# Performance work log

Measured on AMD Instinct MI355X. Metric: run time of the kernel, lower is better.

The kernel has to match this reference:

```python
import jax, jax.numpy as jnp
import numpy as np

D = 1024      # embedding_dimension
F = 4096      # intermediate_dimension
E = 8         # num_experts
K = 2         # top_k
B, S = 4, 2048


def setup_inputs() -> dict:
    key = jax.random.key(0)
    ks = jax.random.split(key, 6)
    scale_in = 1.0 / np.sqrt(D)
    scale_mid = 1.0 / np.sqrt(F)
    return {
        "x": jax.random.normal(ks[0], (B, S, D), dtype=jnp.float32),
        "router_w": jax.random.normal(ks[1], (E, D), dtype=jnp.float32) * scale_in,   # nn.Linear weight [out,in]
        "w1": jax.random.normal(ks[2], (E, F, D), dtype=jnp.float32) * scale_in,
        "b1": jax.random.normal(ks[3], (E, F), dtype=jnp.float32) * 0.01,
        "w2": jax.random.normal(ks[4], (E, D, F), dtype=jnp.float32) * scale_mid,
        "b2": jax.random.normal(ks[5], (E, D), dtype=jnp.float32) * 0.01,
    }


def reference(x, router_w, w1, b1, w2, b2):
    orig_shape = x.shape
    xf = x.reshape(-1, D)                                  # [T, D]
    logits = jnp.einsum("td,ed->te", xf, router_w)        # [T, E]
    top_vals, top_idx = jax.lax.top_k(logits, K)           # [T, K]
    probs = jax.nn.softmax(top_vals, axis=-1)              # [T, K]

    out = jnp.zeros_like(xf)
    for e in range(E):  # small fixed expert loop; masked dense combine
        # combine weight per token for expert e (0 if not routed)
        w = jnp.sum(jnp.where(top_idx == e, probs, 0.0), axis=-1)   # [T]
        h = jax.nn.gelu(jnp.einsum("td,fd->tf", xf, w1[e]) + b1[e], approximate=False)
        y = jnp.einsum("tf,df->td", h, w2[e]) + b2[e]
        out = out + w[:, None] * y
    return out.reshape(orig_shape)
```

## Files before the change

kernel.cpp:

```cpp
#include <hip/hip_runtime.h>
#include <hip/hip_bf16.h>
#include <stdint.h>

#define D 1024
#define F 4096
#define E 8
#define T 8192
#define SLOT_CAP 18432
#define BM 128
#define BK 32
#define EP_STRIDE 136

#define BM2 256
#define BN2 256
#define BK2 32
#define EP2 268

typedef __attribute__((ext_vector_type(8))) short bf16x8;
typedef __attribute__((ext_vector_type(4))) float f32x4;
typedef __attribute__((ext_vector_type(8))) unsigned short u16x8;

__device__ __forceinline__ unsigned short f2bf(float f) {
  unsigned u = __float_as_uint(f);
  u += 0x7fffu + ((u >> 16) & 1u);
  return (unsigned short)(u >> 16);
}
__device__ __forceinline__ float bf2f(unsigned short u) {
  return __uint_as_float(((unsigned)u) << 16);
}

__device__ __forceinline__ float gelu_f(float v) {
  float s = fabsf(v) * 0.70710678118654752f;
  float t = __builtin_amdgcn_rcpf(fmaf(0.3275911f, s, 1.0f));
  float p = fmaf(t, 1.061405429f, -1.453152027f);
  p = fmaf(t, p, 1.421413741f);
  p = fmaf(t, p, -0.284496736f);
  p = fmaf(t, p, 0.254829592f);
  p = p * t;
  float e = 1.0f - p * __expf(-s * s);
  e = copysignf(e, v);
  return 0.5f * v * (1.0f + e);
}

__device__ __forceinline__ void gload16(const void* g, void* l) {
  auto gp = (const __attribute__((address_space(1))) unsigned int*)(uintptr_t)g;
  auto lp = (__attribute__((address_space(3))) unsigned int*)(unsigned)(uintptr_t)l;
  __builtin_amdgcn_global_load_lds(gp, lp, 16, 0, 0);
}

__global__ __launch_bounds__(256) void prep_kernel(const float* __restrict__ x,
                                                   const float* __restrict__ rw,
                                                   const float* __restrict__ w1,
                                                   const float* __restrict__ w2,
                                                   int* __restrict__ tok_e,
                                                   float* __restrict__ tok_p,
                                                   unsigned short* __restrict__ xg,
                                                   unsigned short* __restrict__ w1g,
                                                   unsigned short* __restrict__ w2g) {
  if (blockIdx.x >= 2048) {
    const int n8 = E * F * D / 8;
    int i = (blockIdx.x - 2048) * 256 + threadIdx.x;
    const float* in = w1;
    unsigned short* out = w1g;
    if (i >= n8) { i -= n8; in = w2; out = w2g; }
    const float4* p = (const float4*)in + (size_t)i * 2;
    float4 a = p[0], b = p[1];
    u16x8 o;
    o[0] = f2bf(a.x); o[1] = f2bf(a.y); o[2] = f2bf(a.z); o[3] = f2bf(a.w);
    o[4] = f2bf(b.x); o[5] = f2bf(b.y); o[6] = f2bf(b.z); o[7] = f2bf(b.w);
    *(u16x8*)(out + (size_t)i * 8) = o;
    return;
  }
  int t = blockIdx.x * 4 + (threadIdx.x >> 6);
  int lane = threadIdx.x & 63;
  const float* xp = x + (size_t)t * D;
  unsigned short* xgp = xg + (size_t)t * D;
  double acc[E];
#pragma unroll
  for (int e = 0; e < E; e++) acc[e] = 0.0;
  for (int j = 0; j < D / 64; j++) {
    float xv = xp[j * 64 + lane];
    xgp[j * 64 + lane] = f2bf(xv);
#pragma unroll
    for (int e = 0; e < E; e++) acc[e] += (double)xv * (double)rw[e * D + j * 64 + lane];
  }
#pragma unroll
  for (int e = 0; e < E; e++) {
#pragma unroll
    for (int off = 32; off >= 1; off >>= 1) acc[e] += __shfl_xor(acc[e], off, 64);
  }
  if (lane == 0) {
    double v0 = -1e300, v1 = -1e300;
    int i0 = 0, i1 = 0;
#pragma unroll
    for (int e = 0; e < E; e++) {
      double v = acc[e];
      if (v > v0) { v1 = v0; i1 = i0; v0 = v; i0 = e; }
      else if (v > v1) { v1 = v; i1 = e; }
    }
    double e1 = exp(v1 - v0);
    double s = 1.0 + e1;
    tok_e[2 * t] = i0; tok_e[2 * t + 1] = i1;
    tok_p[2 * t] = (float)(1.0 / s);
    tok_p[2 * t + 1] = (float)(e1 / s);
  }
}

__global__ __launch_bounds__(64) void bucket_kernel(const int* __restrict__ tok_e,
                                                    int* __restrict__ perm,
                                                    int* __restrict__ slot_of,
                                                    int* __restrict__ counts,
                                                    int* __restrict__ offp) {
  const int e = blockIdx.x;
  const int lane = threadIdx.x;
  int cnt[E];
#pragma unroll
  for (int ee = 0; ee < E; ee++) cnt[ee] = 0;
  for (int idx = lane; idx < 2 * T; idx += 64) {
    int v = tok_e[idx];
#pragma unroll
    for (int ee = 0; ee < E; ee++) cnt[ee] += (v == ee) ? 1 : 0;
  }
#pragma unroll
  for (int ee = 0; ee < E; ee++) {
#pragma unroll
    for (int off = 32; off >= 1; off >>= 1) cnt[ee] += __shfl_xor(cnt[ee], off, 64);
  }
  int off_e[E + 1];
  int o = 0;
#pragma unroll
  for (int ee = 0; ee < E; ee++) { off_e[ee] = o; o += (cnt[ee] + 255) & ~255; }
  off_e[E] = o;
  if (e == 0 && lane == 0) {
#pragma unroll
    for (int ee = 0; ee < E; ee++) { counts[ee] = cnt[ee]; offp[ee] = off_e[ee]; }
    offp[E] = o;
  }
  int base = 0, mycnt = 0, myend = 0;
#pragma unroll
  for (int ee = 0; ee < E; ee++) {
    if (ee == e) { base = off_e[ee]; mycnt = cnt[ee]; myend = off_e[ee + 1]; }
  }
  const int pad0 = base + mycnt;
  for (int r = 0; r < 2 * T / 64; r++) {
    int idx = r * 64 + lane;
    int v = tok_e[idx];
    bool m = (v == e);
    unsigned long long mask = __ballot(m);
    int pre = __popcll(mask & ((1ull << lane) - 1ull));
    if (m) {
      int slot = base + pre;
      perm[slot] = idx >> 1;
      slot_of[idx] = slot;
    }
    base += __popcll(mask);
  }
  for (int i = pad0 + lane; i < myend; i += 64) perm[i] = 0;
}

__global__ __launch_bounds__(512, 2) void gemm1_kernel(const unsigned short* __restrict__ xg,
                                                       const unsigned short* __restrict__ w1g,
                                                       const float* __restrict__ b1,
                                                       const int* __restrict__ perm,
                                                       const int* __restrict__ offp,
                                                       const int* __restrict__ counts,
                                                       unsigned short* __restrict__ hbuf) {
  const int id = blockIdx.x;
  const int swz = (id & 7) * 144 + (id >> 3);
  const int bm = swz >> 4, bn = swz & 15;
  const int row0 = bm * BM2;
  if (row0 >= offp[E]) return;
  int e = 0;
#pragma unroll
  for (int i = 0; i < E; i++) if (row0 >= offp[i + 1]) e = i + 1;
  if (row0 >= offp[e] + counts[e]) return;

  const int t = threadIdx.x, lane = t & 63, w = t >> 6;
  const int wm = w >> 2, wn = w & 3;
  const int fr = lane & 15, fq = lane >> 4;

  __shared__ __align__(16) unsigned short smem[65536];

  const int srow = t >> 2;
  const int c = (t & 3) ^ (srow & 3);
  const unsigned short* srcA[2];
  const unsigned short* srcB[2];
  {
    int p0 = perm[row0 + srow], p1 = perm[row0 + 128 + srow];
    srcA[0] = xg + (size_t)p0 * D + c * 8;
    srcA[1] = xg + (size_t)p1 * D + c * 8;
    srcB[0] = w1g + ((size_t)e * F + (size_t)bn * BN2 + srow) * D + c * 8;
    srcB[1] = w1g + ((size_t)e * F + (size_t)bn * BN2 + 128 + srow) * D + c * 8;
  }

  float biasv[4];
#pragma unroll
  for (int n = 0; n < 4; n++) {
    biasv[n] = b1[e * F + bn * BN2 + wn * 64 + n * 16 + fr];
    asm volatile("" :: "v"(biasv[n]));
  }

  auto stageA = [&](int tk) {
    unsigned short* base = smem + (tk & 3) * 16384 + t * 8;
    gload16(srcA[0] + tk * 32, base);
    gload16(srcA[1] + tk * 32, base + 4096);
  };
  auto stageB = [&](int tk) {
    unsigned short* base = smem + (tk & 3) * 16384 + 8192 + t * 8;
    gload16(srcB[0] + tk * 32, base);
    gload16(srcB[1] + tk * 32, base + 4096);
  };

  int aoff[8], boff[4];
#pragma unroll
  for (int m = 0; m < 8; m++) {
    int row = wm * 128 + m * 16 + fr;
    aoff[m] = row * 32 + ((fq ^ (row & 3)) * 8);
  }
#pragma unroll
  for (int n = 0; n < 4; n++) {
    int row = wn * 64 + n * 16 + fr;
    boff[n] = 8192 + row * 32 + ((fq ^ (row & 3)) * 8);
  }

  f32x4 acc[8][4] = {};

  stageA(0); stageB(0);
  stageA(1); stageB(1);
  stageA(2); stageB(2);
  asm volatile("s_waitcnt vmcnt(8)" ::: "memory");
  __builtin_amdgcn_s_barrier();
  __builtin_amdgcn_sched_barrier(0);

  const int NK = D / BK2;
#pragma unroll 4
  for (int kt = 0; kt < NK; ++kt) {
    const unsigned short* tb = smem + (kt & 3) * 16384;
    bf16x8 a0[4], b[4];
#pragma unroll
    for (int m = 0; m < 4; m++) a0[m] = *(const bf16x8*)(tb + aoff[m]);
#pragma unroll
    for (int n = 0; n < 4; n++) b[n] = *(const bf16x8*)(tb + boff[n]);
    if (kt + 3 < NK) stageA(kt + 3);
    __builtin_amdgcn_s_setprio(1);
#pragma unroll
    for (int m = 0; m < 4; m++)
#pragma unroll
      for (int n = 0; n < 4; n++)
        acc[m][n] = __builtin_amdgcn_mfma_f32_16x16x32_bf16(a0[m], b[n], acc[m][n], 0, 0, 0);
    __builtin_amdgcn_s_setprio(0);
    __builtin_amdgcn_s_barrier();
    __builtin_amdgcn_sched_barrier(0);
    bf16x8 a1[4];
#pragma unroll
    for (int m = 0; m < 4; m++) a1[m] = *(const bf16x8*)(tb + aoff[4 + m]);
    if (kt + 3 < NK) stageB(kt + 3);
    __builtin_amdgcn_s_setprio(1);
#pragma unroll
    for (int m = 0; m < 4; m++)
#pragma unroll
      for (int n = 0; n < 4; n++)
        acc[4 + m][n] = __builtin_amdgcn_mfma_f32_16x16x32_bf16(a1[m], b[n], acc[4 + m][n], 0, 0, 0);
    __builtin_amdgcn_s_setprio(0);
    if (kt < NK - 3)       { asm volatile("s_waitcnt vmcnt(8)" ::: "memory"); }
    else if (kt == NK - 3) { asm volatile("s_waitcnt vmcnt(4)" ::: "memory"); }
    else if (kt == NK - 2) { asm volatile("s_waitcnt vmcnt(0)" ::: "memory"); }
    __builtin_amdgcn_s_barrier();
    __builtin_amdgcn_sched_barrier(0);
  }

  __syncthreads();
  unsigned short* ep = smem;
#pragma unroll
  for (int p = 0; p < 2; p++) {
    if (wm == p) {
#pragma unroll
      for (int n = 0; n < 4; n++) {
        int col = wn * 64 + n * 16 + fr;
#pragma unroll
        for (int m = 0; m < 8; m++) {
#pragma unroll
          for (int j = 0; j < 4; j++) {
            int lr = m * 16 + fq * 4 + j;
            ep[lr * EP2 + col] = f2bf(gelu_f(acc[m][n][j] + biasv[n]));
          }
        }
      }
    }
    __syncthreads();
#pragma unroll
    for (int i = 0; i < 8; i++) {
      int idx = t + i * 512;
      int r2 = idx >> 5, c8 = (idx & 31) * 8;
      u16x8 v = *(const u16x8*)&ep[r2 * EP2 + c8];
      *(u16x8*)&hbuf[(size_t)(row0 + p * 128 + r2) * F + (size_t)bn * BN2 + c8] = v;
    }
    __syncthreads();
  }
}

__global__ __launch_bounds__(256, 3) void gemm2_kernel(const unsigned short* __restrict__ hbuf,
                                                       const unsigned short* __restrict__ w2g,
                                                       const float* __restrict__ b2,
                                                       const int* __restrict__ offp,
                                                       const int* __restrict__ counts,
                                                       unsigned short* __restrict__ ypart) {
  const int id = blockIdx.x;
  const int swz = (id & 7) * 288 + (id >> 3);
  const int bn = swz & 7;
  const int ks = (swz >> 3) & 1;
  const int bm = swz >> 4;
  const int row0 = bm * BM;
  if (row0 >= offp[E]) return;
  int e = 0;
#pragma unroll
  for (int i = 0; i < E; i++) if (row0 >= offp[i + 1]) e = i + 1;
  const int valid_end = offp[e] + counts[e];
  if (row0 >= valid_end) return;

  const int tid = threadIdx.x, lane = tid & 63, w = tid >> 6;
  __shared__ __align__(16) unsigned short smem[BM * EP_STRIDE];
  unsigned short* As0 = smem;
  unsigned short* Bs0 = smem + 8192;

  const int kbase = ks * (F / 2);
  const unsigned short* gsrc[4];
  unsigned short* ldst[4];
#pragma unroll
  for (int i = 0; i < 4; i++) {
    int ch = tid + 256 * i;
    if (ch < 512) {
      int ar = ch >> 2, ac = (ch & 3) * 8;
      gsrc[i] = hbuf + (size_t)(row0 + ar) * F + kbase + ac;
      ldst[i] = As0 + ch * 8;
    } else {
      int c = ch - 512;
      int br = c >> 2, bc = (c & 3) * 8;
      gsrc[i] = w2g + ((size_t)e * D + (size_t)bn * BM + br) * F + kbase + bc;
      ldst[i] = Bs0 + c * 8;
    }
  }
  auto stage = [&](int k0, int buf) {
#pragma unroll
    for (int i = 0; i < 4; i++) gload16(gsrc[i] + k0, ldst[i] + buf * (BM * BK));
  };

  f32x4 acc[4][4] = {};
  const int wr = (w >> 1) * 64, wc = (w & 1) * 64;
  const int fr = lane & 15, fq = lane >> 4;

  stage(0, 0);
  __syncthreads();
  int cur = 0;
  for (int k0 = 0; k0 < F / 2; k0 += BK) {
    if (k0 + BK < F / 2) stage(k0 + BK, cur ^ 1);
    bf16x8 a[4], b[4];
#pragma unroll
    for (int m = 0; m < 4; m++) a[m] = *(const bf16x8*)&As0[cur * 4096 + (wr + m * 16 + fr) * BK + fq * 8];
#pragma unroll
    for (int n = 0; n < 4; n++) b[n] = *(const bf16x8*)&Bs0[cur * 4096 + (wc + n * 16 + fr) * BK + fq * 8];
#pragma unroll
    for (int m = 0; m < 4; m++)
#pragma unroll
      for (int n = 0; n < 4; n++)
        acc[m][n] = __builtin_amdgcn_mfma_f32_16x16x32_bf16(a[m], b[n], acc[m][n], 0, 0, 0);
    __syncthreads();
    cur ^= 1;
  }

#pragma unroll
  for (int n = 0; n < 4; n++) {
    int cl = wc + n * 16 + fr;
    float bias = (ks == 0) ? b2[e * D + bn * BM + cl] : 0.0f;
#pragma unroll
    for (int m = 0; m < 4; m++) {
#pragma unroll
      for (int j = 0; j < 4; j++) {
        int rl = wr + m * 16 + fq * 4 + j;
        smem[rl * EP_STRIDE + cl] = f2bf(acc[m][n][j] + bias);
      }
    }
  }
  __syncthreads();
  unsigned short* ybase = ypart + (size_t)ks * SLOT_CAP * D;
#pragma unroll
  for (int i = 0; i < 8; i++) {
    int idx = tid + i * 256;
    int r2 = idx >> 4, c = (idx & 15) * 8;
    if (row0 + r2 < valid_end) {
      u16x8 v = *(const u16x8*)&smem[r2 * EP_STRIDE + c];
      *(u16x8*)&ybase[(size_t)(row0 + r2) * D + bn * BM + c] = v;
    }
  }
}

__global__ __launch_bounds__(256) void combine_kernel(const unsigned short* __restrict__ ypart,
                                                      const int* __restrict__ slot_of,
                                                      const float* __restrict__ tok_p,
                                                      float* __restrict__ out) {
  int i = blockIdx.x * 256 + threadIdx.x;
  int t = i >> 7;
  int g8 = i & 127;
  int s0 = slot_of[2 * t], s1 = slot_of[2 * t + 1];
  float g0 = tok_p[2 * t], g1 = tok_p[2 * t + 1];
  const unsigned short* p0 = ypart;
  const unsigned short* p1 = ypart + (size_t)SLOT_CAP * D;
  u16x8 a0 = *(const u16x8*)(p0 + (size_t)s0 * D + g8 * 8);
  u16x8 b0 = *(const u16x8*)(p1 + (size_t)s0 * D + g8 * 8);
  u16x8 a1 = *(const u16x8*)(p0 + (size_t)s1 * D + g8 * 8);
  u16x8 b1 = *(const u16x8*)(p1 + (size_t)s1 * D + g8 * 8);
  float o[8];
#pragma unroll
  for (int j = 0; j < 8; j++)
    o[j] = g0 * (bf2f(a0[j]) + bf2f(b0[j])) + g1 * (bf2f(a1[j]) + bf2f(b1[j]));
  float4* op = (float4*)(out + (size_t)t * D + g8 * 8);
  op[0] = make_float4(o[0], o[1], o[2], o[3]);
  op[1] = make_float4(o[4], o[5], o[6], o[7]);
}

extern "C" void kernel_launch(void* const* d_in, const int* in_sizes, int n_in,
                              void* d_out, int out_size, void* d_ws, size_t ws_size,
                              hipStream_t stream) {
  const float* x = (const float*)d_in[0];
  const float* rw = (const float*)d_in[1];
  const float* w1 = (const float*)d_in[2];
  const float* b1 = (const float*)d_in[3];
  const float* w2 = (const float*)d_in[4];
  const float* b2 = (const float*)d_in[5];
  float* out = (float*)d_out;

  char* ws = (char*)d_ws;
  size_t off = 0;
  auto alloc = [&](size_t bytes) {
    void* p = ws + off;
    off = (off + bytes + 255) & ~(size_t)255;
    return p;
  };
  int* counts = (int*)alloc(E * 4);
  int* offp = (int*)alloc((E + 1) * 4);
  int* tok_e = (int*)alloc((size_t)T * 2 * 4);
  float* tok_p = (float*)alloc((size_t)T * 2 * 4);
  int* perm = (int*)alloc((size_t)SLOT_CAP * 4);
  int* slot_of = (int*)alloc((size_t)T * 2 * 4);
  unsigned short* xg = (unsigned short*)alloc((size_t)T * D * 2);
  unsigned short* w1g = (unsigned short*)alloc((size_t)E * F * D * 2);
  unsigned short* w2g = (unsigned short*)alloc((size_t)E * D * F * 2);
  unsigned short* hbuf = (unsigned short*)alloc((size_t)SLOT_CAP * F * 2);
  unsigned short* ypart = xg;
  (void)ws_size; (void)in_sizes; (void)n_in; (void)out_size;

  hipLaunchKernelGGL(prep_kernel, dim3(2048 + 2 * E * F * D / 8 / 256), dim3(256), 0, stream,
                     x, rw, w1, w2, tok_e, tok_p, xg, w1g, w2g);
  hipLaunchKernelGGL(bucket_kernel, dim3(E), dim3(64), 0, stream,
                     tok_e, perm, slot_of, counts, offp);
  hipLaunchKernelGGL(gemm1_kernel, dim3(1152), dim3(512), 0, stream,
                     xg, w1g, b1, perm, offp, counts, hbuf);
  hipLaunchKernelGGL(gemm2_kernel, dim3(2304), dim3(256), 0, stream,
                     hbuf, w2g, b2, offp, counts, ypart);
  hipLaunchKernelGGL(combine_kernel, dim3(T * D / 8 / 256), dim3(256), 0, stream,
                     ypart, slot_of, tok_p, out);
}
```

Before: 626.8 us.

## Overlap w2 bf16 conversion with gemm1 and shrink its LDS pipeline to three stages

Moves the w2 fp32-to-bf16 conversion out of prep_kernel and into extra trailing blocks of gemm1, so the conversion runs alongside the GEMM instead of before it. The gemm1 main loop drops from a four-buffer to a three-buffer LDS ring, adds barriers and lgkmcnt waits, changes the LDS swizzle pattern and the epilogue pitch, and reduces shared memory from 128KB to 96KB. The aim is to hide the weight conversion bandwidth behind compute and to allow more resident blocks per CU. The cost is a shallower prefetch and extra barriers inside the loop.

```diff
diff --git a/kernel.cpp b/kernel.cpp
--- a/kernel.cpp
+++ b/kernel.cpp
@@ -13,8 +13,7 @@
 
 #define BM2 256
 #define BN2 256
-#define BK2 32
-#define EP2 268
+#define EP2 264
 
 typedef __attribute__((ext_vector_type(8))) short bf16x8;
 typedef __attribute__((ext_vector_type(4))) float f32x4;
@@ -51,24 +50,18 @@
 __global__ __launch_bounds__(256) void prep_kernel(const float* __restrict__ x,
                                                    const float* __restrict__ rw,
                                                    const float* __restrict__ w1,
-                                                   const float* __restrict__ w2,
                                                    int* __restrict__ tok_e,
                                                    float* __restrict__ tok_p,
                                                    unsigned short* __restrict__ xg,
-                                                   unsigned short* __restrict__ w1g,
-                                                   unsigned short* __restrict__ w2g) {
+                                                   unsigned short* __restrict__ w1g) {
   if (blockIdx.x >= 2048) {
-    const int n8 = E * F * D / 8;
     int i = (blockIdx.x - 2048) * 256 + threadIdx.x;
-    const float* in = w1;
-    unsigned short* out = w1g;
-    if (i >= n8) { i -= n8; in = w2; out = w2g; }
-    const float4* p = (const float4*)in + (size_t)i * 2;
+    const float4* p = (const float4*)w1 + (size_t)i * 2;
     float4 a = p[0], b = p[1];
     u16x8 o;
     o[0] = f2bf(a.x); o[1] = f2bf(a.y); o[2] = f2bf(a.z); o[3] = f2bf(a.w);
     o[4] = f2bf(b.x); o[5] = f2bf(b.y); o[6] = f2bf(b.z); o[7] = f2bf(b.w);
-    *(u16x8*)(out + (size_t)i * 8) = o;
+    *(u16x8*)(w1g + (size_t)i * 8) = o;
     return;
   }
   int t = blockIdx.x * 4 + (threadIdx.x >> 6);
@@ -164,8 +157,22 @@
                                                        const int* __restrict__ perm,
                                                        const int* __restrict__ offp,
                                                        const int* __restrict__ counts,
-                                                       unsigned short* __restrict__ hbuf) {
+                                                       unsigned short* __restrict__ hbuf,
+                                                       const float* __restrict__ w2,
+                                                       unsigned short* __restrict__ w2g) {
   const int id = blockIdx.x;
+  if (id >= 1152) {
+    int i = (id - 1152) * 512 + threadIdx.x;
+    if (i < E * D * F / 8) {
+      const float4* p = (const float4*)w2 + (size_t)i * 2;
+      float4 a = p[0], b = p[1];
+      u16x8 o;
+      o[0] = f2bf(a.x); o[1] = f2bf(a.y); o[2] = f2bf(a.z); o[3] = f2bf(a.w);
+      o[4] = f2bf(b.x); o[5] = f2bf(b.y); o[6] = f2bf(b.z); o[7] = f2bf(b.w);
+      *(u16x8*)(w2g + (size_t)i * 8) = o;
+    }
+    return;
+  }
   const int swz = (id & 7) * 144 + (id >> 3);
   const int bm = swz >> 4, bn = swz & 15;
   const int row0 = bm * BM2;
@@ -179,34 +186,24 @@
   const int wm = w >> 2, wn = w & 3;
   const int fr = lane & 15, fq = lane >> 4;
 
-  __shared__ __align__(16) unsigned short smem[65536];
+  __shared__ __align__(16) unsigned short smem[49152];
 
   const int srow = t >> 2;
-  const int c = (t & 3) ^ (srow & 3);
+  const int c = (t & 3) ^ ((t >> 3) & 3);
   const unsigned short* srcA[2];
   const unsigned short* srcB[2];
-  {
-    int p0 = perm[row0 + srow], p1 = perm[row0 + 128 + srow];
-    srcA[0] = xg + (size_t)p0 * D + c * 8;
-    srcA[1] = xg + (size_t)p1 * D + c * 8;
-    srcB[0] = w1g + ((size_t)e * F + (size_t)bn * BN2 + srow) * D + c * 8;
-    srcB[1] = w1g + ((size_t)e * F + (size_t)bn * BN2 + 128 + srow) * D + c * 8;
-  }
-
-  float biasv[4];
-#pragma unroll
-  for (int n = 0; n < 4; n++) {
-    biasv[n] = b1[e * F + bn * BN2 + wn * 64 + n * 16 + fr];
-    asm volatile("" :: "v"(biasv[n]));
-  }
-
-  auto stageA = [&](int tk) {
-    unsigned short* base = smem + (tk & 3) * 16384 + t * 8;
+  srcA[0] = xg + (size_t)perm[row0 + srow] * D + c * 8;
+  srcA[1] = xg + (size_t)perm[row0 + 128 + srow] * D + c * 8;
+  srcB[0] = w1g + ((size_t)e * F + (size_t)bn * BN2 + srow) * D + c * 8;
+  srcB[1] = w1g + ((size_t)e * F + (size_t)bn * BN2 + 128 + srow) * D + c * 8;
+
+  auto stageA = [&](int tk, int bufi) {
+    unsigned short* base = smem + bufi * 16384 + t * 8;
     gload16(srcA[0] + tk * 32, base);
     gload16(srcA[1] + tk * 32, base + 4096);
   };
-  auto stageB = [&](int tk) {
-    unsigned short* base = smem + (tk & 3) * 16384 + 8192 + t * 8;
+  auto stageB = [&](int tk, int bufi) {
+    unsigned short* base = smem + bufi * 16384 + 8192 + t * 8;
     gload16(srcB[0] + tk * 32, base);
     gload16(srcB[1] + tk * 32, base + 4096);
   };
@@ -215,62 +212,68 @@
 #pragma unroll
   for (int m = 0; m < 8; m++) {
     int row = wm * 128 + m * 16 + fr;
-    aoff[m] = row * 32 + ((fq ^ (row & 3)) * 8);
+    aoff[m] = row * 32 + ((fq ^ ((row >> 1) & 3)) * 8);
   }
 #pragma unroll
   for (int n = 0; n < 4; n++) {
     int row = wn * 64 + n * 16 + fr;
-    boff[n] = 8192 + row * 32 + ((fq ^ (row & 3)) * 8);
+    boff[n] = 8192 + row * 32 + ((fq ^ ((row >> 1) & 3)) * 8);
   }
 
   f32x4 acc[8][4] = {};
 
-  stageA(0); stageB(0);
-  stageA(1); stageB(1);
-  stageA(2); stageB(2);
-  asm volatile("s_waitcnt vmcnt(8)" ::: "memory");
+  stageA(0, 0); stageB(0, 0);
+  stageA(1, 1); stageB(1, 1);
+  asm volatile("s_waitcnt vmcnt(4)" ::: "memory");
   __builtin_amdgcn_s_barrier();
   __builtin_amdgcn_sched_barrier(0);
 
-  const int NK = D / BK2;
-#pragma unroll 4
+  const int NK = D / BK;
+  int cur = 0, stg = 2;
   for (int kt = 0; kt < NK; ++kt) {
-    const unsigned short* tb = smem + (kt & 3) * 16384;
-    bf16x8 a0[4], b[4];
-#pragma unroll
-    for (int m = 0; m < 4; m++) a0[m] = *(const bf16x8*)(tb + aoff[m]);
+    const unsigned short* tb = smem + cur * 16384;
+    bf16x8 a[4], b[4];
+#pragma unroll
+    for (int m = 0; m < 4; m++) a[m] = *(const bf16x8*)(tb + aoff[m]);
 #pragma unroll
     for (int n = 0; n < 4; n++) b[n] = *(const bf16x8*)(tb + boff[n]);
-    if (kt + 3 < NK) stageA(kt + 3);
+    if (kt + 2 < NK) stageA(kt + 2, stg);
+    __builtin_amdgcn_s_barrier();
+    asm volatile("s_waitcnt lgkmcnt(0)" ::: "memory");
+    __builtin_amdgcn_sched_barrier(0);
     __builtin_amdgcn_s_setprio(1);
 #pragma unroll
     for (int m = 0; m < 4; m++)
 #pragma unroll
       for (int n = 0; n < 4; n++)
-        acc[m][n] = __builtin_amdgcn_mfma_f32_16x16x32_bf16(a0[m], b[n], acc[m][n], 0, 0, 0);
+        acc[m][n] = __builtin_amdgcn_mfma_f32_16x16x32_bf16(a[m], b[n], acc[m][n], 0, 0, 0);
     __builtin_amdgcn_s_setprio(0);
+    bf16x8 a2[4];
+#pragma unroll
+    for (int m = 0; m < 4; m++) a2[m] = *(const bf16x8*)(tb + aoff[4 + m]);
+    if (kt + 2 < NK) stageB(kt + 2, stg);
+    __builtin_amdgcn_s_barrier();
+    asm volatile("s_waitcnt lgkmcnt(0)" ::: "memory");
+    __builtin_amdgcn_sched_barrier(0);
+    __builtin_amdgcn_s_setprio(1);
+#pragma unroll
+    for (int m = 0; m < 4; m++)
+#pragma unroll
+      for (int n = 0; n < 4; n++)
+        acc[4 + m][n] = __builtin_amdgcn_mfma_f32_16x16x32_bf16(a2[m], b[n], acc[4 + m][n], 0, 0, 0);
+    __builtin_amdgcn_s_setprio(0);
+    if (kt < NK - 2) { asm volatile("s_waitcnt vmcnt(4)" ::: "memory"); }
+    else             { asm volatile("s_waitcnt vmcnt(0)" ::: "memory"); }
     __builtin_amdgcn_s_barrier();
     __builtin_amdgcn_sched_barrier(0);
-    bf16x8 a1[4];
-#pragma unroll
-    for (int m = 0; m < 4; m++) a1[m] = *(const bf16x8*)(tb + aoff[4 + m]);
-    if (kt + 3 < NK) stageB(kt + 3);
-    __builtin_amdgcn_s_setprio(1);
-#pragma unroll
-    for (int m = 0; m < 4; m++)
-#pragma unroll
-      for (int n = 0; n < 4; n++)
-        acc[4 + m][n] = __builtin_amdgcn_mfma_f32_16x16x32_bf16(a1[m], b[n], acc[4 + m][n], 0, 0, 0);
-    __builtin_amdgcn_s_setprio(0);
-    if (kt < NK - 3)       { asm volatile("s_waitcnt vmcnt(8)" ::: "memory"); }
-    else if (kt == NK - 3) { asm volatile("s_waitcnt vmcnt(4)" ::: "memory"); }
-    else if (kt == NK - 2) { asm volatile("s_waitcnt vmcnt(0)" ::: "memory"); }
-    __builtin_amdgcn_s_barrier();
-    __builtin_amdgcn_sched_barrier(0);
-  }
-
+    cur = (cur == 2) ? 0 : cur + 1;
+    stg = (stg == 2) ? 0 : stg + 1;
+  }
+
+  float biasv[4];
+#pragma unroll
+  for (int n = 0; n < 4; n++) biasv[n] = b1[e * F + bn * BN2 + wn * 64 + n * 16 + fr];
   __syncthreads();
-  unsigned short* ep = smem;
 #pragma unroll
   for (int p = 0; p < 2; p++) {
     if (wm == p) {
@@ -282,7 +285,7 @@
 #pragma unroll
           for (int j = 0; j < 4; j++) {
             int lr = m * 16 + fq * 4 + j;
-            ep[lr * EP2 + col] = f2bf(gelu_f(acc[m][n][j] + biasv[n]));
+            smem[lr * EP2 + col] = f2bf(gelu_f(acc[m][n][j] + biasv[n]));
           }
         }
       }
@@ -292,7 +295,7 @@
     for (int i = 0; i < 8; i++) {
       int idx = t + i * 512;
       int r2 = idx >> 5, c8 = (idx & 31) * 8;
-      u16x8 v = *(const u16x8*)&ep[r2 * EP2 + c8];
+      u16x8 v = *(const u16x8*)&smem[r2 * EP2 + c8];
       *(u16x8*)&hbuf[(size_t)(row0 + p * 128 + r2) * F + (size_t)bn * BN2 + c8] = v;
     }
     __syncthreads();
@@ -449,12 +452,12 @@
   unsigned short* ypart = xg;
   (void)ws_size; (void)in_sizes; (void)n_in; (void)out_size;
 
-  hipLaunchKernelGGL(prep_kernel, dim3(2048 + 2 * E * F * D / 8 / 256), dim3(256), 0, stream,
-                     x, rw, w1, w2, tok_e, tok_p, xg, w1g, w2g);
+  hipLaunchKernelGGL(prep_kernel, dim3(2048 + E * F * D / 8 / 256), dim3(256), 0, stream,
+                     x, rw, w1, tok_e, tok_p, xg, w1g);
   hipLaunchKernelGGL(bucket_kernel, dim3(E), dim3(64), 0, stream,
                      tok_e, perm, slot_of, counts, offp);
-  hipLaunchKernelGGL(gemm1_kernel, dim3(1152), dim3(512), 0, stream,
-                     xg, w1g, b1, perm, offp, counts, hbuf);
+  hipLaunchKernelGGL(gemm1_kernel, dim3(1152 + E * D * F / 8 / 512), dim3(512), 0, stream,
+                     xg, w1g, b1, perm, offp, counts, hbuf, w2, w2g);
   hipLaunchKernelGGL(gemm2_kernel, dim3(2304), dim3(256), 0, stream,
                      hbuf, w2g, b2, offp, counts, ypart);
   hipLaunchKernelGGL(combine_kernel, dim3(T * D / 8 / 256), dim3(256), 0, stream,
```

Result: faster. 597.6 us (-4.7%).
